# Kernel tuning notes

Measured on AMD Instinct MI355X. Metric: run time of the kernel, lower is better.

Reference implementation:

```python
import math
import jax, jax.numpy as jnp
import numpy as np

S = 2048
D_MOD = 1024
D_K = 64
D_V = 64
H = 16
MASKED = True


def setup_inputs() -> dict:
    key = jax.random.key(0)
    ks = jax.random.split(key, 11)
    sc_in = 1.0 / math.sqrt(D_MOD)
    sc_o = 1.0 / math.sqrt(H * D_V)
    return {
        "Q_input": jax.random.normal(ks[0], (S, D_MOD), jnp.float32),
        "K_input": jax.random.normal(ks[1], (S, D_MOD), jnp.float32),
        "V_input": jax.random.normal(ks[2], (S, D_MOD), jnp.float32),
        # stacked per-head Linear params (torch Linear: y = x @ W.T + b)
        "WQw": jax.random.uniform(ks[3], (H, D_K, D_MOD), jnp.float32, -sc_in, sc_in),
        "WQb": jax.random.uniform(ks[4], (H, D_K), jnp.float32, -sc_in, sc_in),
        "WKw": jax.random.uniform(ks[5], (H, D_K, D_MOD), jnp.float32, -sc_in, sc_in),
        "WKb": jax.random.uniform(ks[6], (H, D_K), jnp.float32, -sc_in, sc_in),
        "WVw": jax.random.uniform(ks[7], (H, D_V, D_MOD), jnp.float32, -sc_in, sc_in),
        "WVb": jax.random.uniform(ks[8], (H, D_V), jnp.float32, -sc_in, sc_in),
        "WOw": jax.random.uniform(ks[9], (D_MOD, H * D_V), jnp.float32, -sc_o, sc_o),
        "WOb": jax.random.uniform(ks[10], (D_MOD,), jnp.float32, -sc_o, sc_o),
    }


def reference(Q_input, K_input, V_input, WQw, WQb, WKw, WKb, WVw, WVb, WOw, WOb):
    # per-head projections, batched over heads: [H, S, d]
    q = jnp.einsum("sd,hkd->hsk", Q_input, WQw) + WQb[:, None, :]
    k = jnp.einsum("sd,hkd->hsk", K_input, WKw) + WKb[:, None, :]
    v = jnp.einsum("sd,hvd->hsv", V_input, WVw) + WVb[:, None, :]
    # raw scores [H, S, T]
    qk = jnp.einsum("hsk,htk->hst", q, k)
    if MASKED:
        qk = jnp.tril(qk)  # torch.tril: zero (not -inf) upper triangle
    # torch log_softmax(dim=0) on each [S, T] matrix -> axis 1 of [H, S, T]
    scores = jax.nn.log_softmax(qk / math.sqrt(D_K), axis=1)
    attn = jnp.einsum("hst,htv->hsv", scores, v)  # [H, S, d_v]
    # torch.cat(head_attns, dim=1) -> [S, H*d_v], head-major feature order
    Z = jnp.transpose(attn, (1, 0, 2)).reshape(S, H * D_V)
    return Z @ WOw.T + WOb
```

## Files before the change

kernel.cpp:

```cpp
#include <hip/hip_runtime.h>
#include <math.h>
#include <stdint.h>

#define S 2048
#define DMOD 1024
#define H 16

typedef unsigned short ushort_t;
typedef short bf16x8 __attribute__((ext_vector_type(8)));
typedef float f32x4 __attribute__((ext_vector_type(4)));

#define SW(r) ((((r) & 7)) ^ ((((r) >> 3) & 3) << 1))

__device__ __forceinline__ ushort_t f2b(float f) {
    union { float f; unsigned u; } x; x.f = f;
    return (ushort_t)((x.u + 0x7FFFu + ((x.u >> 16) & 1u)) >> 16);
}
__device__ __forceinline__ ushort_t f2b_fast(float f) {
    union { float f; unsigned u; } x; x.f = f;
    return (ushort_t)((x.u + 0x8000u) >> 16);
}
__device__ __forceinline__ float b2f(ushort_t b) {
    union { unsigned u; float f; } x; x.u = ((unsigned)b) << 16;
    return x.f;
}
__device__ __forceinline__ void gld16(const ushort_t* g, ushort_t* l) {
    __builtin_amdgcn_global_load_lds(
        (const __attribute__((address_space(1))) unsigned int*)g,
        (__attribute__((address_space(3))) unsigned int*)l, 16, 0, 0);
}

__global__ __launch_bounds__(256) void init_all(
    float* __restrict__ attn_raw, float* __restrict__ out,
    float* __restrict__ sumexp, float* __restrict__ corr)
{
    const int b = blockIdx.x;
    const float4 z4 = {0.f, 0.f, 0.f, 0.f};
    if (b < 2048) {
        *(float4*)(attn_raw + ((size_t)b * 256 + threadIdx.x) * 4) = z4;
    } else if (b < 4096) {
        *(float4*)(out + ((size_t)(b - 2048) * 256 + threadIdx.x) * 4) = z4;
    } else if (b < 4128) {
        int e = ((b - 4096) * 256 + threadIdx.x) * 4;
        float4 v = {(float)(e & 2047), (float)((e + 1) & 2047),
                    (float)((e + 2) & 2047), (float)((e + 3) & 2047)};
        *(float4*)(sumexp + e) = v;
    } else {
        *(float4*)(corr + threadIdx.x * 4) = z4;
    }
}

__global__ __launch_bounds__(256) void convert_all(
    const float* q, const float* k, const float* v,
    const float* wq, const float* wk, const float* wv, const float* wo,
    ushort_t* qo, ushort_t* ko, ushort_t* vo,
    ushort_t* wqo, ushort_t* wko, ushort_t* wvo, ushort_t* woo)
{
    const int seg = blockIdx.y;
    const float* src; ushort_t* dst; size_t off = 0;
    const size_t M1 = (size_t)1 << 20;
    if (seg < 2)       { src = q;  dst = qo;  off = (size_t)seg * M1; }
    else if (seg < 4)  { src = k;  dst = ko;  off = (size_t)(seg - 2) * M1; }
    else if (seg < 6)  { src = v;  dst = vo;  off = (size_t)(seg - 4) * M1; }
    else if (seg == 6) { src = wq; dst = wqo; }
    else if (seg == 7) { src = wk; dst = wko; }
    else if (seg == 8) { src = wv; dst = wvo; }
    else               { src = wo; dst = woo; }
    size_t i = off + ((size_t)blockIdx.x * 256 + threadIdx.x) * 4;
    float4 f = *(const float4*)(src + i);
    union { uint2 u2; ushort_t us[4]; } o;
    o.us[0] = f2b(f.x); o.us[1] = f2b(f.y); o.us[2] = f2b(f.z); o.us[3] = f2b(f.w);
    *(uint2*)(dst + i) = o.u2;
}

__global__ __launch_bounds__(256) void gemm_qkv(
    const ushort_t* __restrict__ A0, const ushort_t* __restrict__ A1,
    const ushort_t* __restrict__ A2, const ushort_t* __restrict__ Wqkv,
    const float* __restrict__ b0, const float* __restrict__ b1,
    const float* __restrict__ b2,
    ushort_t* __restrict__ qbb, ushort_t* __restrict__ kbb,
    ushort_t* __restrict__ vt)
{
    __shared__ ushort_t As[128 * 64];
    __shared__ ushort_t Bs[64 * 64];
    const int tid = threadIdx.x;
    const int lane = tid & 63, wid = tid >> 6;
    const int quad = lane >> 4, l15 = lane & 15;
    const int wr = wid >> 1, wc = wid & 1;
    const int m0 = blockIdx.y * 128;
    const int n0 = blockIdx.x * 64;
    const int seg = n0 >> 10;
    const int nloc = n0 & 1023;
    const ushort_t* A = seg == 0 ? A0 : (seg == 1 ? A1 : A2);
    const float* bias = seg == 0 ? b0 : (seg == 1 ? b1 : b2);

    const f32x4 fz = {0.f, 0.f, 0.f, 0.f};
    f32x4 acc[4][2];
#pragma unroll
    for (int i = 0; i < 4; ++i) { acc[i][0] = fz; acc[i][1] = fz; }

    for (int k0 = 0; k0 < DMOD; k0 += 64) {
        __syncthreads();
#pragma unroll
        for (int i = 0; i < 4; ++i) {
            int c = i * 256 + tid, row = c >> 3, kcl = c & 7;
            gld16(A + (size_t)(m0 + row) * DMOD + k0 + (kcl ^ SW(row)) * 8, &As[c * 8]);
        }
#pragma unroll
        for (int i = 0; i < 2; ++i) {
            int c = i * 256 + tid, row = c >> 3, kcl = c & 7;
            gld16(Wqkv + (size_t)(n0 + row) * DMOD + k0 + (kcl ^ SW(row)) * 8, &Bs[c * 8]);
        }
        __syncthreads();
#pragma unroll
        for (int kc = 0; kc < 2; ++kc) {
            bf16x8 af[4], bfr[2];
#pragma unroll
            for (int mi = 0; mi < 4; ++mi) {
                int row = wr * 64 + mi * 16 + l15;
                af[mi] = *(const bf16x8*)&As[row * 64 + ((kc * 4 + quad) ^ SW(row)) * 8];
            }
#pragma unroll
            for (int ni = 0; ni < 2; ++ni) {
                int row = wc * 32 + ni * 16 + l15;
                bfr[ni] = *(const bf16x8*)&Bs[row * 64 + ((kc * 4 + quad) ^ SW(row)) * 8];
            }
#pragma unroll
            for (int mi = 0; mi < 4; ++mi)
#pragma unroll
                for (int ni = 0; ni < 2; ++ni)
                    acc[mi][ni] = __builtin_amdgcn_mfma_f32_16x16x32_bf16(
                        af[mi], bfr[ni], acc[mi][ni], 0, 0, 0);
        }
    }

    if (seg < 2) {
        ushort_t* C = seg == 0 ? qbb : kbb;
#pragma unroll
        for (int mi = 0; mi < 4; ++mi)
#pragma unroll
            for (int ni = 0; ni < 2; ++ni) {
                int gn = nloc + wc * 32 + ni * 16 + l15;
                float bv = bias[gn];
#pragma unroll
                for (int r = 0; r < 4; ++r) {
                    int gm = m0 + wr * 64 + mi * 16 + quad * 4 + r;
                    C[(size_t)gm * DMOD + gn] = f2b(acc[mi][ni][r] + bv);
                }
            }
    } else {
#pragma unroll
        for (int mi = 0; mi < 4; ++mi)
#pragma unroll
            for (int ni = 0; ni < 2; ++ni) {
                int gn = nloc + wc * 32 + ni * 16 + l15;
                float bv = bias[gn];
                int gmb = m0 + wr * 64 + mi * 16 + quad * 4;
                union { uint2 u2; ushort_t us[4]; } o;
#pragma unroll
                for (int r = 0; r < 4; ++r) o.us[r] = f2b(acc[mi][ni][r] + bv);
                *(uint2*)&vt[(size_t)gn * S + gmb] = o.u2;
            }
    }
}

__global__ __launch_bounds__(512, 4) void attn_mfma(
    const ushort_t* __restrict__ qb, const ushort_t* __restrict__ kb,
    const ushort_t* __restrict__ vt, float* __restrict__ attn_raw,
    float* __restrict__ sumexp)
{
    __shared__ ushort_t QPs[128 * 64];
    __shared__ ushort_t Ks[2][4096];
    __shared__ ushort_t Vs[2][4096];
    __shared__ float    sacc[1024];

    const int h = blockIdx.y;
    const int bx = blockIdx.x;
    const int si = (h < 8) ? (15 - (bx >> 1)) : (bx >> 1);
    const int z = bx & 1;
    const int half = si + 1;
    const int tbeg = z ? half : 0;
    const int tend = z ? 2 * si + 2 : half;
    const int s0 = si * 128;

    const int tid = threadIdx.x;
    const int lane = tid & 63, w = tid >> 6;
    const int quad = lane >> 4, l15 = lane & 15;
    const int sband = s0 + w * 16;

    const ushort_t* qh = qb + h * 64;
    const ushort_t* kh = kb + h * 64;
    const ushort_t* vh = vt + (size_t)(h * 64) * S;

#pragma unroll
    for (int i = 0; i < 2; ++i) {
        int c = i * 512 + tid, row = c >> 3, kcl = c & 7;
        gld16(qh + (size_t)(s0 + row) * DMOD + (kcl ^ SW(row)) * 8, &QPs[c * 8]);
    }
    {
        int t0 = tbeg * 64;
        int row = tid >> 3, kcl = tid & 7;
        gld16(kh + (size_t)(t0 + row) * DMOD + (kcl ^ SW(row)) * 8, &Ks[0][tid * 8]);
        gld16(vh + (size_t)row * S + t0 + (kcl ^ SW(row)) * 8, &Vs[0][tid * 8]);
    }
    for (int i = tid; i < 1024; i += 512) sacc[i] = 0.f;
    __syncthreads();

    bf16x8 aq[2];
    {
        int rq = w * 16 + l15;
#pragma unroll
        for (int kc = 0; kc < 2; ++kc)
            aq[kc] = *(const bf16x8*)&QPs[rq * 64 + ((kc * 4 + quad) ^ SW(rq)) * 8];
    }

    const f32x4 fz = {0.f, 0.f, 0.f, 0.f};
    f32x4 oacc[4];
#pragma unroll
    for (int ni = 0; ni < 4; ++ni) oacc[ni] = fz;
    bool any_live = false;

    for (int it = tbeg; it < tend; ++it) {
        const int p = (it - tbeg) & 1;
        const int t0 = it * 64;
        if (it + 1 < tend) {
            int t1 = t0 + 64;
            int row = tid >> 3, kcl = tid & 7;
            gld16(kh + (size_t)(t1 + row) * DMOD + (kcl ^ SW(row)) * 8, &Ks[1 - p][tid * 8]);
            gld16(vh + (size_t)row * S + t1 + (kcl ^ SW(row)) * 8, &Vs[1 - p][tid * 8]);
        }

        if (t0 < sband + 16) {
            any_live = true;
            f32x4 xf[4];
#pragma unroll
            for (int ti = 0; ti < 4; ++ti) xf[ti] = fz;
#pragma unroll
            for (int kc = 0; kc < 2; ++kc) {
#pragma unroll
                for (int ti = 0; ti < 4; ++ti) {
                    int rk = ti * 16 + l15;
                    bf16x8 bk = *(const bf16x8*)&Ks[p][rk * 64 + ((kc * 4 + quad) ^ SW(rk)) * 8];
                    xf[ti] = __builtin_amdgcn_mfma_f32_16x16x32_bf16(aq[kc], bk, xf[ti], 0, 0, 0);
                }
            }

            const bool clean = (t0 + 63 <= sband);
            const int s_q = sband + quad * 4;
#pragma unroll
            for (int ti = 0; ti < 4; ++ti) {
                int t_g = t0 + ti * 16 + l15;
                float es = 0.f;
                if (clean) {
#pragma unroll
                    for (int r = 0; r < 4; ++r) {
                        float xv = xf[ti][r] * 0.125f;
                        es += __expf(xv);
                        xf[ti][r] = xv;
                    }
                } else {
#pragma unroll
                    for (int r = 0; r < 4; ++r) {
                        float xv = xf[ti][r] * 0.125f;
                        bool live = (s_q + r >= t_g);
                        xv = live ? xv : 0.f;
                        es += live ? __expf(xv) : 0.f;
                        xf[ti][r] = xv;
                    }
                }
                es += __shfl_xor(es, 16, 64);
                es += __shfl_xor(es, 32, 64);
                if (quad == 0) atomicAdd(&sacc[(it - tbeg) * 64 + ti * 16 + l15], es);
#pragma unroll
                for (int r = 0; r < 4; ++r) {
                    int sl = w * 16 + quad * 4 + r;
                    int tc = ti * 16 + l15;
                    QPs[sl * 64 + ((tc >> 3) ^ SW(sl)) * 8 + (tc & 7)] = f2b_fast(xf[ti][r]);
                }
            }

#pragma unroll
            for (int kc = 0; kc < 2; ++kc) {
                int rp = w * 16 + l15;
                bf16x8 ap = *(const bf16x8*)&QPs[rp * 64 + ((kc * 4 + quad) ^ SW(rp)) * 8];
#pragma unroll
                for (int ni = 0; ni < 4; ++ni) {
                    int rv = ni * 16 + l15;
                    bf16x8 bv = *(const bf16x8*)&Vs[p][rv * 64 + ((kc * 4 + quad) ^ SW(rv)) * 8];
                    oacc[ni] = __builtin_amdgcn_mfma_f32_16x16x32_bf16(ap, bv, oacc[ni], 0, 0, 0);
                }
            }
        }
        __syncthreads();
    }

    {
        int nv = (tend - tbeg) * 64;
        for (int i = tid; i < nv; i += 512)
            atomicAdd(&sumexp[h * S + tbeg * 64 + i], sacc[i]);
    }
    if (any_live) {
#pragma unroll
        for (int ni = 0; ni < 4; ++ni)
#pragma unroll
            for (int r = 0; r < 4; ++r) {
                int s_g = s0 + w * 16 + quad * 4 + r;
                atomicAdd(&attn_raw[(size_t)s_g * DMOD + h * 64 + ni * 16 + l15],
                          oacc[ni][r]);
            }
    }
}

__global__ __launch_bounds__(256) void corr_kernel(
    const float* __restrict__ sumexp, const ushort_t* __restrict__ vt,
    float* __restrict__ corr)
{
    const int w = threadIdx.x >> 6, lane = threadIdx.x & 63;
    const int r = blockIdx.x * 4 + w;
    const int h = r >> 6;
    float acc = 0.f;
#pragma unroll
    for (int i = 0; i < 4; ++i) {
        int t = i * 512 + lane * 8;
        bf16x8 vv = *(const bf16x8*)&vt[(size_t)r * S + t];
        float4 s0 = *(const float4*)&sumexp[h * S + t];
        float4 s1 = *(const float4*)&sumexp[h * S + t + 4];
        acc += logf(s0.x) * b2f((ushort_t)vv[0]) + logf(s0.y) * b2f((ushort_t)vv[1])
             + logf(s0.z) * b2f((ushort_t)vv[2]) + logf(s0.w) * b2f((ushort_t)vv[3])
             + logf(s1.x) * b2f((ushort_t)vv[4]) + logf(s1.y) * b2f((ushort_t)vv[5])
             + logf(s1.z) * b2f((ushort_t)vv[6]) + logf(s1.w) * b2f((ushort_t)vv[7]);
    }
#pragma unroll
    for (int d = 1; d < 64; d <<= 1) acc += __shfl_xor(acc, d, 64);
    if (lane == 0) corr[r] = acc;
}

__global__ __launch_bounds__(256) void convert_Z(
    const float* __restrict__ attn_raw, const float* __restrict__ corr,
    ushort_t* __restrict__ Zb)
{
    size_t i = ((size_t)blockIdx.x * 256 + threadIdx.x) * 4;
    float4 f = *(const float4*)(attn_raw + i);
    int c = (int)(i & (DMOD - 1));
    union { uint2 u2; ushort_t us[4]; } o;
    o.us[0] = f2b(f.x - corr[c]);
    o.us[1] = f2b(f.y - corr[c + 1]);
    o.us[2] = f2b(f.z - corr[c + 2]);
    o.us[3] = f2b(f.w - corr[c + 3]);
    *(uint2*)(Zb + i) = o.u2;
}

__global__ __launch_bounds__(256) void gemm_out(
    const ushort_t* __restrict__ A, const ushort_t* __restrict__ W,
    const float* __restrict__ bias, float* __restrict__ C)
{
    __shared__ ushort_t As[128 * 64];
    __shared__ ushort_t Bs[64 * 64];
    const int tid = threadIdx.x;
    const int lane = tid & 63, wid = tid >> 6;
    const int quad = lane >> 4, l15 = lane & 15;
    const int wr = wid >> 1, wc = wid & 1;
    const int m0 = blockIdx.y * 128, n0 = blockIdx.x * 64;
    const int kbeg = blockIdx.z * 512, kend = kbeg + 512;

    const f32x4 fz = {0.f, 0.f, 0.f, 0.f};
    f32x4 acc[4][2];
#pragma unroll
    for (int i = 0; i < 4; ++i) { acc[i][0] = fz; acc[i][1] = fz; }

    for (int k0 = kbeg; k0 < kend; k0 += 64) {
        __syncthreads();
#pragma unroll
        for (int i = 0; i < 4; ++i) {
            int c = i * 256 + tid, row = c >> 3, kcl = c & 7;
            gld16(A + (size_t)(m0 + row) * DMOD + k0 + (kcl ^ SW(row)) * 8, &As[c * 8]);
        }
#pragma unroll
        for (int i = 0; i < 2; ++i) {
            int c = i * 256 + tid, row = c >> 3, kcl = c & 7;
            gld16(W + (size_t)(n0 + row) * DMOD + k0 + (kcl ^ SW(row)) * 8, &Bs[c * 8]);
        }
        __syncthreads();
#pragma unroll
        for (int kc = 0; kc < 2; ++kc) {
            bf16x8 af[4], bfr[2];
#pragma unroll
            for (int mi = 0; mi < 4; ++mi) {
                int row = wr * 64 + mi * 16 + l15;
                af[mi] = *(const bf16x8*)&As[row * 64 + ((kc * 4 + quad) ^ SW(row)) * 8];
            }
#pragma unroll
            for (int ni = 0; ni < 2; ++ni) {
                int row = wc * 32 + ni * 16 + l15;
                bfr[ni] = *(const bf16x8*)&Bs[row * 64 + ((kc * 4 + quad) ^ SW(row)) * 8];
            }
#pragma unroll
            for (int mi = 0; mi < 4; ++mi)
#pragma unroll
                for (int ni = 0; ni < 2; ++ni)
                    acc[mi][ni] = __builtin_amdgcn_mfma_f32_16x16x32_bf16(
                        af[mi], bfr[ni], acc[mi][ni], 0, 0, 0);
        }
    }
#pragma unroll
    for (int mi = 0; mi < 4; ++mi)
#pragma unroll
        for (int ni = 0; ni < 2; ++ni) {
            int gn = n0 + wc * 32 + ni * 16 + l15;
            float bv = (kbeg == 0) ? bias[gn] : 0.f;
#pragma unroll
            for (int r = 0; r < 4; ++r) {
                int gm = m0 + wr * 64 + mi * 16 + quad * 4 + r;
                atomicAdd(&C[(size_t)gm * DMOD + gn], acc[mi][ni][r] + bv);
            }
        }
}

extern "C" void kernel_launch(void* const* d_in, const int* in_sizes, int n_in,
                              void* d_out, int out_size, void* d_ws, size_t ws_size,
                              hipStream_t stream) {
    const float* Qin = (const float*)d_in[0];
    const float* Kin = (const float*)d_in[1];
    const float* Vin = (const float*)d_in[2];
    const float* WQw = (const float*)d_in[3];
    const float* WQb = (const float*)d_in[4];
    const float* WKw = (const float*)d_in[5];
    const float* WKb = (const float*)d_in[6];
    const float* WVw = (const float*)d_in[7];
    const float* WVb = (const float*)d_in[8];
    const float* WOw = (const float*)d_in[9];
    const float* WOb = (const float*)d_in[10];

    float* ws = (float*)d_ws;
    const size_t M1 = (size_t)1 << 20;
    ushort_t* qbb  = (ushort_t*)(ws);
    ushort_t* kbb  = (ushort_t*)(ws + M1);
    ushort_t* vt   = (ushort_t*)(ws + 2 * M1);
    ushort_t* wqkv = (ushort_t*)(ws + 3 * M1);
    ushort_t* wob  = (ushort_t*)(ws + 4 * M1 + M1 / 2);
    ushort_t* Qbin = (ushort_t*)(ws + 5 * M1);
    ushort_t* Kbin = (ushort_t*)(ws + 6 * M1);
    ushort_t* Vbin = (ushort_t*)(ws + 7 * M1);
    float* attn_raw = ws + 6 * M1;
    ushort_t* Zb    = (ushort_t*)(ws + 5 * M1);
    float* sumexp   = ws + 8 * M1;
    float* corr     = ws + 8 * M1 + H * S;

    init_all<<<4129, 256, 0, stream>>>(attn_raw, (float*)d_out, sumexp, corr);

    convert_all<<<dim3(1024, 10), 256, 0, stream>>>(
        Qin, Kin, Vin, WQw, WKw, WVw, WOw,
        Qbin, Kbin, Vbin,
        wqkv, wqkv + (size_t)1024 * 1024, wqkv + (size_t)2 * 1024 * 1024, wob);

    gemm_qkv<<<dim3(48, 16), 256, 0, stream>>>(
        Qbin, Kbin, Vbin, wqkv, WQb, WKb, WVb, qbb, kbb, vt);

    attn_mfma<<<dim3(32, H), 512, 0, stream>>>(qbb, kbb, vt, attn_raw, sumexp);

    corr_kernel<<<256, 256, 0, stream>>>(sumexp, vt, corr);
    convert_Z<<<2048, 256, 0, stream>>>(attn_raw, corr, Zb);

    gemm_out<<<dim3(16, 16, 2), 256, 0, stream>>>(Zb, wob, WOb, (float*)d_out);
}
```

Before: 189.1 us.

## Fuse init into convert kernel, enlarge QKV GEMM tile, cache logs in corr

The zero-init kernel is merged into the bf16 conversion launch as extra grid rows, and attn_raw is moved to a separate workspace region so it no longer aliases the inputs being converted. The QKV projection GEMM switches to 128x128 tiles with 512 threads to improve operand reuse. The correction kernel computes log(sumexp) once per head into shared memory instead of per row. Risks include the larger GEMM tile using more registers and LDS, which can lower occupancy, and the use of the faster approximate __logf.

```diff
diff --git a/kernel.cpp b/kernel.cpp
--- a/kernel.cpp
+++ b/kernel.cpp
@@ -30,33 +30,32 @@
         (__attribute__((address_space(3))) unsigned int*)l, 16, 0, 0);
 }
 
-__global__ __launch_bounds__(256) void init_all(
-    float* __restrict__ attn_raw, float* __restrict__ out,
-    float* __restrict__ sumexp, float* __restrict__ corr)
-{
-    const int b = blockIdx.x;
-    const float4 z4 = {0.f, 0.f, 0.f, 0.f};
-    if (b < 2048) {
-        *(float4*)(attn_raw + ((size_t)b * 256 + threadIdx.x) * 4) = z4;
-    } else if (b < 4096) {
-        *(float4*)(out + ((size_t)(b - 2048) * 256 + threadIdx.x) * 4) = z4;
-    } else if (b < 4128) {
-        int e = ((b - 4096) * 256 + threadIdx.x) * 4;
-        float4 v = {(float)(e & 2047), (float)((e + 1) & 2047),
-                    (float)((e + 2) & 2047), (float)((e + 3) & 2047)};
-        *(float4*)(sumexp + e) = v;
-    } else {
-        *(float4*)(corr + threadIdx.x * 4) = z4;
-    }
-}
-
-__global__ __launch_bounds__(256) void convert_all(
+__global__ __launch_bounds__(256) void prep_all(
     const float* q, const float* k, const float* v,
     const float* wq, const float* wk, const float* wv, const float* wo,
     ushort_t* qo, ushort_t* ko, ushort_t* vo,
-    ushort_t* wqo, ushort_t* wko, ushort_t* wvo, ushort_t* woo)
+    ushort_t* wqo, ushort_t* wko, ushort_t* wvo, ushort_t* woo,
+    float* __restrict__ attn_raw, float* __restrict__ out,
+    float* __restrict__ sumexp, float* __restrict__ corr)
 {
     const int seg = blockIdx.y;
+    const int bx = blockIdx.x;
+    if (seg >= 10) {
+        const float4 z4 = {0.f, 0.f, 0.f, 0.f};
+        if (seg < 12) {
+            *(float4*)(attn_raw + (((size_t)(seg - 10) * 1024 + bx) * 256 + threadIdx.x) * 4) = z4;
+        } else if (seg < 14) {
+            *(float4*)(out + (((size_t)(seg - 12) * 1024 + bx) * 256 + threadIdx.x) * 4) = z4;
+        } else if (bx < 32) {
+            int e = (bx * 256 + threadIdx.x) * 4;
+            float4 vv = {(float)(e & 2047), (float)((e + 1) & 2047),
+                         (float)((e + 2) & 2047), (float)((e + 3) & 2047)};
+            *(float4*)(sumexp + e) = vv;
+        } else if (bx == 32) {
+            *(float4*)(corr + threadIdx.x * 4) = z4;
+        }
+        return;
+    }
     const float* src; ushort_t* dst; size_t off = 0;
     const size_t M1 = (size_t)1 << 20;
     if (seg < 2)       { src = q;  dst = qo;  off = (size_t)seg * M1; }
@@ -66,14 +65,14 @@
     else if (seg == 7) { src = wk; dst = wko; }
     else if (seg == 8) { src = wv; dst = wvo; }
     else               { src = wo; dst = woo; }
-    size_t i = off + ((size_t)blockIdx.x * 256 + threadIdx.x) * 4;
+    size_t i = off + ((size_t)bx * 256 + threadIdx.x) * 4;
     float4 f = *(const float4*)(src + i);
     union { uint2 u2; ushort_t us[4]; } o;
     o.us[0] = f2b(f.x); o.us[1] = f2b(f.y); o.us[2] = f2b(f.z); o.us[3] = f2b(f.w);
     *(uint2*)(dst + i) = o.u2;
 }
 
-__global__ __launch_bounds__(256) void gemm_qkv(
+__global__ __launch_bounds__(512, 4) void gemm_qkv(
     const ushort_t* __restrict__ A0, const ushort_t* __restrict__ A1,
     const ushort_t* __restrict__ A2, const ushort_t* __restrict__ Wqkv,
     const float* __restrict__ b0, const float* __restrict__ b1,
@@ -82,13 +81,13 @@
     ushort_t* __restrict__ vt)
 {
     __shared__ ushort_t As[128 * 64];
-    __shared__ ushort_t Bs[64 * 64];
+    __shared__ ushort_t Bs[128 * 64];
     const int tid = threadIdx.x;
     const int lane = tid & 63, wid = tid >> 6;
     const int quad = lane >> 4, l15 = lane & 15;
-    const int wr = wid >> 1, wc = wid & 1;
+    const int wr = wid >> 2, wc = wid & 3;
     const int m0 = blockIdx.y * 128;
-    const int n0 = blockIdx.x * 64;
+    const int n0 = blockIdx.x * 128;
     const int seg = n0 >> 10;
     const int nloc = n0 & 1023;
     const ushort_t* A = seg == 0 ? A0 : (seg == 1 ? A1 : A2);
@@ -102,13 +101,13 @@
     for (int k0 = 0; k0 < DMOD; k0 += 64) {
         __syncthreads();
 #pragma unroll
-        for (int i = 0; i < 4; ++i) {
-            int c = i * 256 + tid, row = c >> 3, kcl = c & 7;
+        for (int i = 0; i < 2; ++i) {
+            int c = i * 512 + tid, row = c >> 3, kcl = c & 7;
             gld16(A + (size_t)(m0 + row) * DMOD + k0 + (kcl ^ SW(row)) * 8, &As[c * 8]);
         }
 #pragma unroll
         for (int i = 0; i < 2; ++i) {
-            int c = i * 256 + tid, row = c >> 3, kcl = c & 7;
+            int c = i * 512 + tid, row = c >> 3, kcl = c & 7;
             gld16(Wqkv + (size_t)(n0 + row) * DMOD + k0 + (kcl ^ SW(row)) * 8, &Bs[c * 8]);
         }
         __syncthreads();
@@ -315,24 +314,30 @@
     const float* __restrict__ sumexp, const ushort_t* __restrict__ vt,
     float* __restrict__ corr)
 {
-    const int w = threadIdx.x >> 6, lane = threadIdx.x & 63;
-    const int r = blockIdx.x * 4 + w;
-    const int h = r >> 6;
-    float acc = 0.f;
-#pragma unroll
-    for (int i = 0; i < 4; ++i) {
-        int t = i * 512 + lane * 8;
-        bf16x8 vv = *(const bf16x8*)&vt[(size_t)r * S + t];
-        float4 s0 = *(const float4*)&sumexp[h * S + t];
-        float4 s1 = *(const float4*)&sumexp[h * S + t + 4];
-        acc += logf(s0.x) * b2f((ushort_t)vv[0]) + logf(s0.y) * b2f((ushort_t)vv[1])
-             + logf(s0.z) * b2f((ushort_t)vv[2]) + logf(s0.w) * b2f((ushort_t)vv[3])
-             + logf(s1.x) * b2f((ushort_t)vv[4]) + logf(s1.y) * b2f((ushort_t)vv[5])
-             + logf(s1.z) * b2f((ushort_t)vv[6]) + logf(s1.w) * b2f((ushort_t)vv[7]);
-    }
-#pragma unroll
-    for (int d = 1; d < 64; d <<= 1) acc += __shfl_xor(acc, d, 64);
-    if (lane == 0) corr[r] = acc;
+    __shared__ float ls[S];
+    const int h = blockIdx.x >> 2;
+    const int r0 = blockIdx.x * 16;
+    const int tid = threadIdx.x;
+    for (int t = tid; t < S; t += 256)
+        ls[t] = __logf(sumexp[h * S + t]);
+    __syncthreads();
+    const int w = tid >> 6, lane = tid & 63;
+#pragma unroll
+    for (int rr = 0; rr < 4; ++rr) {
+        int r = r0 + w * 4 + rr;
+        float acc = 0.f;
+#pragma unroll
+        for (int i = 0; i < 4; ++i) {
+            int t = i * 512 + lane * 8;
+            bf16x8 vv = *(const bf16x8*)&vt[(size_t)r * S + t];
+#pragma unroll
+            for (int j = 0; j < 8; ++j)
+                acc += ls[t + j] * b2f((ushort_t)vv[j]);
+        }
+#pragma unroll
+        for (int d = 1; d < 64; d <<= 1) acc += __shfl_xor(acc, d, 64);
+        if (lane == 0) corr[r] = acc;
+    }
 }
 
 __global__ __launch_bounds__(256) void convert_Z(
@@ -441,24 +446,23 @@
     ushort_t* Qbin = (ushort_t*)(ws + 5 * M1);
     ushort_t* Kbin = (ushort_t*)(ws + 6 * M1);
     ushort_t* Vbin = (ushort_t*)(ws + 7 * M1);
-    float* attn_raw = ws + 6 * M1;
-    ushort_t* Zb    = (ushort_t*)(ws + 5 * M1);
     float* sumexp   = ws + 8 * M1;
     float* corr     = ws + 8 * M1 + H * S;
-
-    init_all<<<4129, 256, 0, stream>>>(attn_raw, (float*)d_out, sumexp, corr);
-
-    convert_all<<<dim3(1024, 10), 256, 0, stream>>>(
+    float* attn_raw = ws + 9 * M1;
+    ushort_t* Zb    = (ushort_t*)(ws + 5 * M1);
+
+    prep_all<<<dim3(1024, 15), 256, 0, stream>>>(
         Qin, Kin, Vin, WQw, WKw, WVw, WOw,
         Qbin, Kbin, Vbin,
-        wqkv, wqkv + (size_t)1024 * 1024, wqkv + (size_t)2 * 1024 * 1024, wob);
-
-    gemm_qkv<<<dim3(48, 16), 256, 0, stream>>>(
+        wqkv, wqkv + (size_t)1024 * 1024, wqkv + (size_t)2 * 1024 * 1024, wob,
+        attn_raw, (float*)d_out, sumexp, corr);
+
+    gemm_qkv<<<dim3(24, 16), 512, 0, stream>>>(
         Qbin, Kbin, Vbin, wqkv, WQb, WKb, WVb, qbb, kbb, vt);
 
     attn_mfma<<<dim3(32, H), 512, 0, stream>>>(qbb, kbb, vt, attn_raw, sumexp);
 
-    corr_kernel<<<256, 256, 0, stream>>>(sumexp, vt, corr);
+    corr_kernel<<<64, 256, 0, stream>>>(sumexp, vt, corr);
     convert_Z<<<2048, 256, 0, stream>>>(attn_raw, corr, Zb);
 
     gemm_out<<<dim3(16, 16, 2), 256, 0, stream>>>(Zb, wob, WOb, (float*)d_out);
```

Result: no change. 189.0 us (-0.1%).
